# Optimization experiments

Measured on AMD Instinct MI355X. Metric: run time of the kernel, lower is better.

The kernel has to match this reference:

```python
import jax, jax.numpy as jnp
import numpy as np

DIST_THRESHOLD = 900.0  # distance_threshold from __init__
NO_CODE_ID = -1         # no_code_id from __init__


def setup_inputs() -> dict:
    key = jax.random.key(0)
    k1, k2 = jax.random.split(key)
    x = jax.random.normal(k1, (4, 2048, 512), dtype=jnp.float32)      # [b, n, d] tokens
    codes = jax.random.normal(k2, (16384, 512), dtype=jnp.float32)    # [c, d] full codebook
    return {"x": x, "codes": codes}


def reference(x, codes):
    x2 = jnp.sum(x * x, axis=-1, keepdims=True)            # [b, n, 1]
    c2 = jnp.sum(codes * codes, axis=-1)                   # [c]
    xc = jnp.einsum('bnd,cd->bnc', x, codes)               # [b, n, c] (the compute-heavy GEMM)
    dist_sq = jnp.maximum(x2 + c2 - 2.0 * xc, 0.0)         # clamp tiny negatives, like cdist

    within = jnp.any(dist_sq <= DIST_THRESHOLD, axis=-1)   # [b, n]
    nn_ids = jnp.argmin(dist_sq, axis=-1)                  # [b, n]
    ids = jnp.where(within, nn_ids, NO_CODE_ID)            # tokens outside threshold -> no_code_id
    return ids
```

## Files before the change

### kernel.cpp

```cpp
#include <hip/hip_runtime.h>


#define NTOK   8192
#define NCODES 16384
#define DDIM   512
#define NCHUNK 8
#define CHUNK  2048
#define DIST_THR 900.0f

typedef unsigned short u16;
typedef _Float16 half8 __attribute__((ext_vector_type(8)));
typedef float    f32x4 __attribute__((ext_vector_type(4)));

__device__ __forceinline__ void conv_body(const float* __restrict__ src,
                                          u16* __restrict__ dh,
                                          u16* __restrict__ dl, int c) {
    int r = c & 15, q = (c >> 4) & 3, g = (c >> 6) & 7, kit = (c >> 9) & 15;
    int tile = c >> 13;
    int row = tile * 128 + g * 16 + r;
    int k = kit * 32 + q * 8;
    const float* p = src + (size_t)row * DDIM + k;
    float4 v0 = *(const float4*)p;
    float4 v1 = *(const float4*)(p + 4);
    float vv[8] = {v0.x, v0.y, v0.z, v0.w, v1.x, v1.y, v1.z, v1.w};
    u16 hs[8], ls[8];
    #pragma unroll
    for (int j = 0; j < 8; ++j) {
        float sv = vv[j] * 16.0f;
        _Float16 h = (_Float16)sv;
        float hf = (float)h;
        _Float16 l = (_Float16)(sv - hf);
        union { _Float16 f; u16 u; } uh, ul;
        uh.f = h; ul.f = l;
        hs[j] = uh.u; ls[j] = ul.u;
    }
    uint4 H, L;
    H.x = hs[0] | ((unsigned)hs[1] << 16); H.y = hs[2] | ((unsigned)hs[3] << 16);
    H.z = hs[4] | ((unsigned)hs[5] << 16); H.w = hs[6] | ((unsigned)hs[7] << 16);
    L.x = ls[0] | ((unsigned)ls[1] << 16); L.y = ls[2] | ((unsigned)ls[3] << 16);
    L.z = ls[4] | ((unsigned)ls[5] << 16); L.w = ls[6] | ((unsigned)ls[7] << 16);
    *(uint4*)(dh + (size_t)c * 8) = H;
    *(uint4*)(dl + (size_t)c * 8) = L;
}

__global__ __launch_bounds__(256) void nn_prep(const float* __restrict__ x,
                                               const float* __restrict__ codes,
                                               u16* __restrict__ xh, u16* __restrict__ xl,
                                               u16* __restrict__ ch, u16* __restrict__ cl,
                                               float* __restrict__ c2) {
    int b = blockIdx.x;
    if (b < 2048) {
        conv_body(x, xh, xl, b * 256 + threadIdx.x);
    } else if (b < 6144) {
        conv_body(codes, ch, cl, (b - 2048) * 256 + threadIdx.x);
    } else {
        int w = threadIdx.x >> 6;
        int lane = threadIdx.x & 63;
        int c = (b - 6144) * 4 + w;
        const float* p = codes + (size_t)c * DDIM + lane * 8;
        float4 v0 = *(const float4*)p;
        float4 v1 = *(const float4*)(p + 4);
        float s = v0.x*v0.x + v0.y*v0.y + v0.z*v0.z + v0.w*v0.w
                + v1.x*v1.x + v1.y*v1.y + v1.z*v1.z + v1.w*v1.w;
        #pragma unroll
        for (int off = 32; off > 0; off >>= 1) s += __shfl_down(s, off);
        if (lane == 0) c2[c] = s;
    }
}

__global__ __launch_bounds__(512, 2) void nn_gemm(const u16* __restrict__ xh,
                                                  const u16* __restrict__ xl,
                                                  const u16* __restrict__ chh,
                                                  const u16* __restrict__ cll,
                                                  const float* __restrict__ c2,
                                                  float* __restrict__ pmin,
                                                  int* __restrict__ pid) {
    __shared__ __align__(16) char smem[131072];
    const int tid = threadIdx.x;
    const int lane = tid & 63;
    const int wave = tid >> 6;
    const int wm = wave & 3;
    const int wn = wave >> 2;
    const int mtile = blockIdx.x >> 3;
    const int chunk = blockIdx.x & 7;
    const int m0 = mtile * 256;

    const int plane = wave >> 1;
    const int tsub  = wave & 1;
    const bool isA = (plane < 2);
    const u16* gbase;
    if (plane == 0)      gbase = xh  + ((size_t)(mtile * 2 + tsub) * 16) * 4096;
    else if (plane == 1) gbase = xl  + ((size_t)(mtile * 2 + tsub) * 16) * 4096;
    else if (plane == 2) gbase = chh + ((size_t)(chunk * 16 + tsub) * 16) * 4096;
    else                 gbase = cll + ((size_t)(chunk * 16 + tsub) * 16) * 4096;
    gbase += lane * 8;
    const int ldsoff = wave * 8192;

    float mv[16];
    int   mi[16];
    #pragma unroll
    for (int s = 0; s < 16; ++s) { mv[s] = 3.4e38f; mi[s] = 0; }

    f32x4 acc[4][8];
    #pragma unroll
    for (int i = 0; i < 4; ++i)
        #pragma unroll
        for (int j = 0; j < 8; ++j) acc[i][j] = (f32x4)0.0f;

    auto stage = [&](int it2) {
        int kit2 = it2 & 15, nt2 = it2 >> 4;
        size_t off = (size_t)(isA ? kit2 : nt2 * 32 + kit2) * 4096;
        const u16* src = gbase + off;
        char* dst = smem + (size_t)(it2 & 1) * 65536 + ldsoff;
        #pragma unroll
        for (int s = 0; s < 8; ++s)
            __builtin_amdgcn_global_load_lds(
                (const __attribute__((address_space(1))) void*)(src + s * 512),
                (__attribute__((address_space(3))) void*)(dst + s * 1024),
                16, 0, 0);
    };

    stage(0);
    for (int it = 0; it < 128; ++it) {
        if (it < 127) {
            stage(it + 1);
            asm volatile("s_waitcnt vmcnt(8)\n\ts_barrier" ::: "memory");
        } else {
            asm volatile("s_waitcnt vmcnt(0)\n\ts_barrier" ::: "memory");
        }

        const char* cur = smem + (size_t)(it & 1) * 65536;
        half8 ah[4], al[4];
        #pragma unroll
        for (int i = 0; i < 4; ++i) {
            int g = wm * 4 + i;
            ah[i] = *(const half8*)(cur +         g * 1024 + lane * 16);
            al[i] = *(const half8*)(cur + 16384 + g * 1024 + lane * 16);
        }
        #pragma unroll
        for (int j = 0; j < 8; ++j) {
            int g = wn * 8 + j;
            half8 bh = *(const half8*)(cur + 32768 + g * 1024 + lane * 16);
            half8 bl = *(const half8*)(cur + 49152 + g * 1024 + lane * 16);
            #pragma unroll
            for (int i = 0; i < 4; ++i) {
                acc[i][j] = __builtin_amdgcn_mfma_f32_16x16x32_f16(ah[i], bh, acc[i][j], 0, 0, 0);
                acc[i][j] = __builtin_amdgcn_mfma_f32_16x16x32_f16(ah[i], bl, acc[i][j], 0, 0, 0);
                acc[i][j] = __builtin_amdgcn_mfma_f32_16x16x32_f16(al[i], bh, acc[i][j], 0, 0, 0);
            }
        }

        if ((it & 15) == 15) {
            int nt = it >> 4;
            #pragma unroll
            for (int j = 0; j < 8; ++j) {
                int ncol = nt * 256 + wn * 128 + j * 16 + (lane & 15);
                int gid = chunk * CHUNK + ncol;
                float cv = c2[gid];
                #pragma unroll
                for (int i = 0; i < 4; ++i)
                    #pragma unroll
                    for (int r = 0; r < 4; ++r) {
                        float s = fmaf(acc[i][j][r], -0.0078125f, cv);
                        int slot = i * 4 + r;
                        if (s < mv[slot]) { mv[slot] = s; mi[slot] = gid; }
                    }
            }
            #pragma unroll
            for (int i = 0; i < 4; ++i)
                #pragma unroll
                for (int j = 0; j < 8; ++j) acc[i][j] = (f32x4)0.0f;
        }
        asm volatile("s_barrier" ::: "memory");
    }

    #pragma unroll
    for (int off = 1; off < 16; off <<= 1) {
        #pragma unroll
        for (int s = 0; s < 16; ++s) {
            float ov = __shfl_xor(mv[s], off);
            int   oi = __shfl_xor(mi[s], off);
            if (ov < mv[s] || (ov == mv[s] && oi < mi[s])) { mv[s] = ov; mi[s] = oi; }
        }
    }
    if ((lane & 15) == 0) {
        #pragma unroll
        for (int i = 0; i < 4; ++i)
            #pragma unroll
            for (int r = 0; r < 4; ++r) {
                int row = wm * 64 + i * 16 + (lane >> 4) * 4 + r;
                int2 e;
                e.x = __float_as_int(mv[i * 4 + r]);
                e.y = mi[i * 4 + r];
                *(int2*)(smem + (wn * 256 + row) * 8) = e;
            }
    }
    __syncthreads();
    if (tid < 256) {
        int2 e0 = *(const int2*)(smem + tid * 8);
        int2 e1 = *(const int2*)(smem + (256 + tid) * 8);
        float v0 = __int_as_float(e0.x), v1 = __int_as_float(e1.x);
        float bv = v0; int bi = e0.y;
        if (v1 < bv || (v1 == bv && e1.y < bi)) { bv = v1; bi = e1.y; }
        pmin[(size_t)(m0 + tid) * NCHUNK + chunk] = bv;
        pid [(size_t)(m0 + tid) * NCHUNK + chunk] = bi;
    }
}

__global__ __launch_bounds__(256) void nn_fin(const float* __restrict__ x,
                                              const float* __restrict__ pmin,
                                              const int* __restrict__ pid,
                                              int* __restrict__ out) {
    int w = threadIdx.x >> 6;
    int lane = threadIdx.x & 63;
    int t = blockIdx.x * 4 + w;
    const float* p = x + (size_t)t * DDIM + lane * 8;
    float4 v0 = *(const float4*)p;
    float4 v1 = *(const float4*)(p + 4);
    float s = v0.x*v0.x + v0.y*v0.y + v0.z*v0.z + v0.w*v0.w
            + v1.x*v1.x + v1.y*v1.y + v1.z*v1.z + v1.w*v1.w;
    #pragma unroll
    for (int off = 32; off > 0; off >>= 1) s += __shfl_down(s, off);
    if (lane == 0) {
        const float* pm = pmin + (size_t)t * NCHUNK;
        const int*   pi = pid  + (size_t)t * NCHUNK;
        float bv = pm[0]; int bi = pi[0];
        #pragma unroll
        for (int c = 1; c < NCHUNK; ++c) {
            float v = pm[c]; int id = pi[c];
            if (v < bv || (v == bv && id < bi)) { bv = v; bi = id; }
        }
        float mind = s + bv;
        out[t] = (mind <= DIST_THR) ? bi : -1;
    }
}

extern "C" void kernel_launch(void* const* d_in, const int* in_sizes, int n_in,
                              void* d_out, int out_size, void* d_ws, size_t ws_size,
                              hipStream_t stream) {
    const float* x     = (const float*)d_in[0];
    const float* codes = (const float*)d_in[1];
    int* out = (int*)d_out;

    char* ws = (char*)d_ws;
    u16*   xh   = (u16*)(ws);
    u16*   xl   = (u16*)(ws + 8388608);
    u16*   chh  = (u16*)(ws + 16777216);
    u16*   cll  = (u16*)(ws + 33554432);
    float* c2   = (float*)(ws + 50331648);
    float* pmin = (float*)(ws + 50397184);
    int*   pid  = (int*)  (ws + 50659328);

    nn_prep<<<10240, 256, 0, stream>>>(x, codes, xh, xl, chh, cll, c2);
    nn_gemm<<<32 * NCHUNK, 512, 0, stream>>>(xh, xl, chh, cll, c2, pmin, pid);
    nn_fin<<<NTOK / 4, 256, 0, stream>>>(x, pmin, pid, out);
}
```

Before: 408.3 us.

## Load MFMA fragments directly from global memory instead of LDS staging

Removes the double-buffered global_load_lds staging pipeline and the per-iteration barriers. Each wave now reads its A and B half8 fragments straight from the pre-swizzled global arrays into registers, and shared memory is cut down to a small reduction buffer. This avoids LDS traffic and block-wide synchronisation. The cost is that waves sharing tiles no longer share them through LDS, so global and L2 traffic rise and latency hiding now relies on the compiler's scheduling inside the unrolled k loop.

```diff
diff --git a/kernel.cpp b/kernel.cpp
--- a/kernel.cpp
+++ b/kernel.cpp
@@ -75,7 +75,7 @@
                                                   const float* __restrict__ c2,
                                                   float* __restrict__ pmin,
                                                   int* __restrict__ pid) {
-    __shared__ __align__(16) char smem[131072];
+    __shared__ __align__(16) char red[4096];
     const int tid = threadIdx.x;
     const int lane = tid & 63;
     const int wave = tid >> 6;
@@ -85,93 +85,66 @@
     const int chunk = blockIdx.x & 7;
     const int m0 = mtile * 256;
 
-    const int plane = wave >> 1;
-    const int tsub  = wave & 1;
-    const bool isA = (plane < 2);
-    const u16* gbase;
-    if (plane == 0)      gbase = xh  + ((size_t)(mtile * 2 + tsub) * 16) * 4096;
-    else if (plane == 1) gbase = xl  + ((size_t)(mtile * 2 + tsub) * 16) * 4096;
-    else if (plane == 2) gbase = chh + ((size_t)(chunk * 16 + tsub) * 16) * 4096;
-    else                 gbase = cll + ((size_t)(chunk * 16 + tsub) * 16) * 4096;
-    gbase += lane * 8;
-    const int ldsoff = wave * 8192;
+    size_t aoff = ((size_t)(mtile * 2 + (wm >> 1)) * 16) * 8192
+                + (size_t)((wm & 1) * 4) * 1024 + (size_t)lane * 16;
+    const char* Ahb = (const char*)xh + aoff;
+    const char* Alb = (const char*)xl + aoff;
 
     float mv[16];
     int   mi[16];
     #pragma unroll
     for (int s = 0; s < 16; ++s) { mv[s] = 3.4e38f; mi[s] = 0; }
 
-    f32x4 acc[4][8];
-    #pragma unroll
-    for (int i = 0; i < 4; ++i)
-        #pragma unroll
-        for (int j = 0; j < 8; ++j) acc[i][j] = (f32x4)0.0f;
-
-    auto stage = [&](int it2) {
-        int kit2 = it2 & 15, nt2 = it2 >> 4;
-        size_t off = (size_t)(isA ? kit2 : nt2 * 32 + kit2) * 4096;
-        const u16* src = gbase + off;
-        char* dst = smem + (size_t)(it2 & 1) * 65536 + ldsoff;
-        #pragma unroll
-        for (int s = 0; s < 8; ++s)
-            __builtin_amdgcn_global_load_lds(
-                (const __attribute__((address_space(1))) void*)(src + s * 512),
-                (__attribute__((address_space(3))) void*)(dst + s * 1024),
-                16, 0, 0);
-    };
-
-    stage(0);
-    for (int it = 0; it < 128; ++it) {
-        if (it < 127) {
-            stage(it + 1);
-            asm volatile("s_waitcnt vmcnt(8)\n\ts_barrier" ::: "memory");
-        } else {
-            asm volatile("s_waitcnt vmcnt(0)\n\ts_barrier" ::: "memory");
-        }
-
-        const char* cur = smem + (size_t)(it & 1) * 65536;
-        half8 ah[4], al[4];
-        #pragma unroll
-        for (int i = 0; i < 4; ++i) {
-            int g = wm * 4 + i;
-            ah[i] = *(const half8*)(cur +         g * 1024 + lane * 16);
-            al[i] = *(const half8*)(cur + 16384 + g * 1024 + lane * 16);
-        }
+    #pragma unroll 1
+    for (int nt = 0; nt < 8; ++nt) {
+        size_t boff = ((size_t)((chunk * 16 + nt * 2 + wn) * 16)) * 8192
+                    + (size_t)lane * 16;
+        const char* Bhb = (const char*)chh + boff;
+        const char* Blb = (const char*)cll + boff;
+
+        f32x4 acc[4][8];
+        #pragma unroll
+        for (int i = 0; i < 4; ++i)
+            #pragma unroll
+            for (int j = 0; j < 8; ++j) acc[i][j] = (f32x4)0.0f;
+
+        #pragma unroll
+        for (int kit = 0; kit < 16; ++kit) {
+            half8 ah[4], al[4], bh[8], bl[8];
+            #pragma unroll
+            for (int i = 0; i < 4; ++i) {
+                ah[i] = *(const half8*)(Ahb + kit * 8192 + i * 1024);
+                al[i] = *(const half8*)(Alb + kit * 8192 + i * 1024);
+            }
+            #pragma unroll
+            for (int j = 0; j < 8; ++j) {
+                bh[j] = *(const half8*)(Bhb + kit * 8192 + j * 1024);
+                bl[j] = *(const half8*)(Blb + kit * 8192 + j * 1024);
+            }
+            #pragma unroll
+            for (int j = 0; j < 8; ++j)
+                #pragma unroll
+                for (int i = 0; i < 4; ++i) {
+                    acc[i][j] = __builtin_amdgcn_mfma_f32_16x16x32_f16(ah[i], bh[j], acc[i][j], 0, 0, 0);
+                    acc[i][j] = __builtin_amdgcn_mfma_f32_16x16x32_f16(ah[i], bl[j], acc[i][j], 0, 0, 0);
+                    acc[i][j] = __builtin_amdgcn_mfma_f32_16x16x32_f16(al[i], bh[j], acc[i][j], 0, 0, 0);
+                }
+        }
+
         #pragma unroll
         for (int j = 0; j < 8; ++j) {
-            int g = wn * 8 + j;
-            half8 bh = *(const half8*)(cur + 32768 + g * 1024 + lane * 16);
-            half8 bl = *(const half8*)(cur + 49152 + g * 1024 + lane * 16);
-            #pragma unroll
-            for (int i = 0; i < 4; ++i) {
-                acc[i][j] = __builtin_amdgcn_mfma_f32_16x16x32_f16(ah[i], bh, acc[i][j], 0, 0, 0);
-                acc[i][j] = __builtin_amdgcn_mfma_f32_16x16x32_f16(ah[i], bl, acc[i][j], 0, 0, 0);
-                acc[i][j] = __builtin_amdgcn_mfma_f32_16x16x32_f16(al[i], bh, acc[i][j], 0, 0, 0);
-            }
-        }
-
-        if ((it & 15) == 15) {
-            int nt = it >> 4;
-            #pragma unroll
-            for (int j = 0; j < 8; ++j) {
-                int ncol = nt * 256 + wn * 128 + j * 16 + (lane & 15);
-                int gid = chunk * CHUNK + ncol;
-                float cv = c2[gid];
-                #pragma unroll
-                for (int i = 0; i < 4; ++i)
-                    #pragma unroll
-                    for (int r = 0; r < 4; ++r) {
-                        float s = fmaf(acc[i][j][r], -0.0078125f, cv);
-                        int slot = i * 4 + r;
-                        if (s < mv[slot]) { mv[slot] = s; mi[slot] = gid; }
-                    }
-            }
+            int ncol = nt * 256 + wn * 128 + j * 16 + (lane & 15);
+            int gid = chunk * CHUNK + ncol;
+            float cv = c2[gid];
             #pragma unroll
             for (int i = 0; i < 4; ++i)
                 #pragma unroll
-                for (int j = 0; j < 8; ++j) acc[i][j] = (f32x4)0.0f;
-        }
-        asm volatile("s_barrier" ::: "memory");
+                for (int r = 0; r < 4; ++r) {
+                    float s = fmaf(acc[i][j][r], -0.0078125f, cv);
+                    int slot = i * 4 + r;
+                    if (s < mv[slot]) { mv[slot] = s; mi[slot] = gid; }
+                }
+        }
     }
 
     #pragma unroll
@@ -192,13 +165,13 @@
                 int2 e;
                 e.x = __float_as_int(mv[i * 4 + r]);
                 e.y = mi[i * 4 + r];
-                *(int2*)(smem + (wn * 256 + row) * 8) = e;
+                *(int2*)(red + (wn * 256 + row) * 8) = e;
             }
     }
     __syncthreads();
     if (tid < 256) {
-        int2 e0 = *(const int2*)(smem + tid * 8);
-        int2 e1 = *(const int2*)(smem + (256 + tid) * 8);
+        int2 e0 = *(const int2*)(red + tid * 8);
+        int2 e1 = *(const int2*)(red + (256 + tid) * 8);
         float v0 = __int_as_float(e0.x), v1 = __int_as_float(e1.x);
         float bv = v0; int bi = e0.y;
         if (v1 < bv || (v1 == bv && e1.y < bi)) { bv = v1; bi = e1.y; }
```

Result: slower. 956.2 us (+134.2%).
